# Performance work log

Measured on AMD Instinct MI355X. Metric: run time of the kernel, lower is better.

The kernel has to match this reference:

```python
import jax, jax.numpy as jnp
import numpy as np

F_FEAT = 310   # len(feature_names)
B = 2048       # samples; x has F_FEAT*B elements
H = 32         # sfp_neurons


def _uniform(key, shape, bound):
    return jax.random.uniform(key, shape, jnp.float32, -bound, bound)


def setup_inputs() -> dict:
    key = jax.random.key(0)
    ks = jax.random.split(key, 7)
    x = jax.random.normal(ks[0], (F_FEAT, B), dtype=jnp.float32)
    # Stacked per-feature MLP params (torch Linear default init: U(-1/sqrt(fan_in), +)).
    s1 = 1.0 / np.sqrt(F_FEAT - 1)
    s2 = 1.0 / np.sqrt(H)
    W1 = _uniform(ks[1], (F_FEAT, F_FEAT - 1, H), s1)  # (in, out) layout
    b1 = _uniform(ks[2], (F_FEAT, H), s1)
    W2 = _uniform(ks[3], (F_FEAT, H, H), s2)
    b2 = _uniform(ks[4], (F_FEAT, H), s2)
    W3 = _uniform(ks[5], (F_FEAT, H, H), s2)
    b3 = _uniform(ks[6], (F_FEAT, H), s2)
    return {"x": x, "W1": W1, "b1": b1, "W2": W2, "b2": b2, "W3": W3, "b3": b3}


def reference(x, W1, b1, W2, b2, W3, b3):
    F_, B_ = x.shape
    # Leave-one-out gather: for SFP i, rows [0..i-1, i+1..F-1] of x (feature-major),
    # then the original's view(-1, 1, F-1) reinterprets the flat buffer as (B, F-1).
    idx = jnp.arange(F_ - 1)[None, :]
    idx = idx + (idx >= jnp.arange(F_)[:, None])          # (F, F-1)
    X = x[idx].reshape(F_, B_, F_ - 1)                    # (F, B, F-1) grouped inputs
    h = jax.nn.relu(jnp.einsum('fbk,fkh->fbh', X, W1) + b1[:, None, :])
    h = jax.nn.relu(jnp.einsum('fbh,fhg->fbg', h, W2) + b2[:, None, :])
    h = jax.nn.relu(jnp.einsum('fbh,fhg->fbg', h, W3) + b3[:, None, :])  # (F, B, H)
    # torch.cat of per-SFP .view(-1) == row-major flatten of (F, B, H)
    return h.reshape(-1)
```

## Files before the change

kernel.cpp:

```cpp
#include <hip/hip_runtime.h>

namespace {

constexpr int F_FEAT = 310;
constexpr int KDIM   = 309;
constexpr int BSZ    = 2048;
constexpr int HDIM   = 32;
constexpr int NCH    = 10;
constexpr int NX     = F_FEAT * BSZ;

constexpr int    NBLK8    = NX / 8 + 2;
constexpr size_t CSTR_B   = (size_t)NBLK8 * 16;
constexpr size_t XC_BYTES = CSTR_B * 8;
constexpr size_t W1T_FSTR = 32 * 320 * 2;
constexpr size_t W1T_OFF  = XC_BYTES;
constexpr size_t W2T_OFF  = W1T_OFF + (size_t)F_FEAT * W1T_FSTR;
constexpr size_t WT_FSTR  = 32 * 32 * 2;
constexpr size_t W3T_OFF  = W2T_OFF + (size_t)F_FEAT * WT_FSTR;
constexpr size_t WS_NEED  = W3T_OFF + (size_t)F_FEAT * WT_FSTR;

constexpr int NBX      = (NBLK8 + 255) / 256;
constexpr int CVT_XBLK = NBX * 8;
constexpr int CVT_BLK  = CVT_XBLK + F_FEAT * 6;

typedef __bf16 bf16x8 __attribute__((ext_vector_type(8)));
typedef float  f32x4  __attribute__((ext_vector_type(4)));

#define MFMA(a, b, c) __builtin_amdgcn_mfma_f32_16x16x32_bf16((a), (b), (c), 0, 0, 0)

__global__ __launch_bounds__(256) void cvt_all(
    const float* __restrict__ x,  const float* __restrict__ W1,
    const float* __restrict__ W2, const float* __restrict__ W3,
    char* __restrict__ ws)
{
    __shared__ float tile[64][33];
    const int b = blockIdx.x, tid = threadIdx.x;

    if (b < CVT_XBLK) {
        const int c = b / NBX, mb = b - c * NBX;
        const int m = mb * 256 + tid;
        if (m >= NBLK8) return;
        const int e0 = m * 8 - c;
        bf16x8 v;
        #pragma unroll
        for (int q = 0; q < 8; ++q) {
            const int i = e0 + q;
            v[q] = (__bf16)((i >= 0 && i < NX) ? x[i] : 0.f);
        }
        *(bf16x8*)(ws + (size_t)c * CSTR_B + (size_t)m * 16) = v;
        return;
    }

    const int wb = b - CVT_XBLK;
    const int fi = wb / 6, part = wb - fi * 6;

    if (part < 5) {
        const float* Wg = W1 + (size_t)fi * KDIM * HDIM;
        const int row = tid >> 2;
        const int c8  = (tid & 3) * 8;
        const int k   = part * 64 + row;
        float4 f0 = make_float4(0,0,0,0), f1 = f0;
        if (k < KDIM) {
            f0 = *(const float4*)&Wg[k * HDIM + c8];
            f1 = *(const float4*)&Wg[k * HDIM + c8 + 4];
        }
        tile[row][c8+0] = f0.x; tile[row][c8+1] = f0.y;
        tile[row][c8+2] = f0.z; tile[row][c8+3] = f0.w;
        tile[row][c8+4] = f1.x; tile[row][c8+5] = f1.y;
        tile[row][c8+6] = f1.z; tile[row][c8+7] = f1.w;
        __syncthreads();
        const int h = tid & 31, kq = (tid >> 5) * 8;
        bf16x8 o;
        #pragma unroll
        for (int j = 0; j < 8; ++j) o[j] = (__bf16)tile[kq + j][h];
        const int boff = (h * 640 + part * 128 + kq * 2) ^ ((h & 7) << 4);
        *(bf16x8*)(ws + W1T_OFF + (size_t)fi * W1T_FSTR + (size_t)boff) = o;
    } else {
        const int kl = tid >> 3, h4 = (tid & 7) * 4;
        const int h = tid & 31, kq = (tid >> 5) * 8;
        {
            const float* Wg = W2 + (size_t)fi * HDIM * HDIM;
            float4 f = *(const float4*)&Wg[kl * HDIM + h4];
            tile[kl][h4+0] = f.x; tile[kl][h4+1] = f.y;
            tile[kl][h4+2] = f.z; tile[kl][h4+3] = f.w;
            __syncthreads();
            if (tid < 128) {
                bf16x8 o;
                #pragma unroll
                for (int j = 0; j < 8; ++j) o[j] = (__bf16)tile[kq + j][h];
                *(bf16x8*)(ws + W2T_OFF + (size_t)fi * WT_FSTR + (size_t)(h * 32 + kq) * 2) = o;
            }
            __syncthreads();
        }
        {
            const float* Wg = W3 + (size_t)fi * HDIM * HDIM;
            float4 f = *(const float4*)&Wg[kl * HDIM + h4];
            tile[kl][h4+0] = f.x; tile[kl][h4+1] = f.y;
            tile[kl][h4+2] = f.z; tile[kl][h4+3] = f.w;
            __syncthreads();
            if (tid < 128) {
                bf16x8 o;
                #pragma unroll
                for (int j = 0; j < 8; ++j) o[j] = (__bf16)tile[kq + j][h];
                *(bf16x8*)(ws + W3T_OFF + (size_t)fi * WT_FSTR + (size_t)(h * 32 + kq) * 2) = o;
            }
        }
    }
}

template<bool FAST>
__global__ __launch_bounds__(256, 4) void sfp5(
    const float* __restrict__ x,
    const float* __restrict__ W1, const float* __restrict__ b1,
    const float* __restrict__ W2, const float* __restrict__ b2,
    const float* __restrict__ W3, const float* __restrict__ b3,
    const char* __restrict__ ws, float* __restrict__ out)
{
    __shared__ __attribute__((aligned(16))) __bf16 W1s[32 * 320];
    __shared__ __attribute__((aligned(16))) __bf16 h1s[256 * 40];

    int fi, sb;
    if (FAST) {
        const int xc = blockIdx.x & 7, li = blockIdx.x >> 3;
        const int cnt = (xc < 6) ? 39 : 38;
        const int lf = li >> 3;
        if (lf >= cnt) return;
        fi = ((xc < 6) ? xc * 39 : 234 + (xc - 6) * 38) + lf;
        sb = li & 7;
    } else {
        fi = blockIdx.x >> 3; sb = blockIdx.x & 7;
    }

    const int tid = threadIdx.x, lane = tid & 63, wv = tid >> 6;
    const int l15 = lane & 15, l16 = lane >> 4;
    const int lk8 = l16 * 8, r0 = l16 * 4;
    const int b0 = sb << 8, iB = fi << 11;
    const int mrow = wv * 64;

    int lin[4];
    const char* base[4];
    #pragma unroll
    for (int m = 0; m < 4; ++m) {
        lin[m] = (b0 + mrow + 16 * m + l15) * KDIM + lk8;
        if (FAST) {
            const int c8 = (-lin[m]) & 7;
            base[m] = ws + (size_t)c8 * CSTR_B + (size_t)(lin[m] + c8) * 2;
        } else {
            base[m] = ws;
        }
    }

    auto fragA = [&](const char* bp, int li_) -> bf16x8 {
        if (FAST) {
            if (__builtin_expect((unsigned)(iB - 1 - li_) < 7u, 0)) {
                bf16x8 r;
                #pragma unroll
                for (int q = 0; q < 8; ++q) {
                    int i = li_ + q; i += (i >= iB) ? BSZ : 0;
                    r[q] = *(const __bf16*)(ws + (size_t)i * 2);
                }
                return r;
            }
            return *(const bf16x8*)(bp + ((li_ >= iB) ? 4096 : 0));
        } else {
            bf16x8 r;
            #pragma unroll
            for (int q = 0; q < 8; ++q) {
                int i = li_ + q; i += (i >= iB) ? BSZ : 0;
                i = (i < NX) ? i : (NX - 1);
                r[q] = (__bf16)x[i];
            }
            return r;
        }
    };

    auto fragW1 = [&](int c, int hrow) -> bf16x8 {
        if (FAST) {
            const int boff = (hrow * 640 + c * 64 + l16 * 16) ^ ((hrow & 7) << 4);
            return *(const bf16x8*)((const char*)W1s + boff);
        } else {
            const float* Wg = W1 + (size_t)fi * KDIM * HDIM;
            bf16x8 r;
            #pragma unroll
            for (int q = 0; q < 8; ++q) {
                const int k = c * 32 + lk8 + q;
                r[q] = (__bf16)((k < KDIM) ? Wg[k * HDIM + hrow] : 0.f);
            }
            return r;
        }
    };

    bf16x8 a0[4], a1[4], a2[4];
    #pragma unroll
    for (int m = 0; m < 4; ++m) a0[m] = fragA(base[m], lin[m]);
    #pragma unroll
    for (int m = 0; m < 4; ++m) a1[m] = fragA(base[m] + 64, lin[m] + 32);

    if (FAST) {
        const char* src = ws + W1T_OFF + (size_t)fi * W1T_FSTR;
        #pragma unroll
        for (int i = 0; i < 5; ++i) {
            const int off = i * 4096 + tid * 16;
            *(bf16x8*)((char*)W1s + off) = *(const bf16x8*)(src + off);
        }
        __syncthreads();
    }

    f32x4 acc[4][2];
    #pragma unroll
    for (int m = 0; m < 4; ++m) { acc[m][0] = {0,0,0,0}; acc[m][1] = {0,0,0,0}; }

    bf16x8 w0 = fragW1(0, l15), w1 = fragW1(0, 16 + l15);
    #pragma unroll
    for (int c = 0; c < NCH; ++c) {
        if (c + 2 < NCH) {
            #pragma unroll
            for (int m = 0; m < 4; ++m)
                a2[m] = fragA(base[m] + 64 * (c + 2), lin[m] + 32 * (c + 2));
        }
        bf16x8 nw0, nw1;
        if (c + 1 < NCH) { nw0 = fragW1(c + 1, l15); nw1 = fragW1(c + 1, 16 + l15); }
        #pragma unroll
        for (int m = 0; m < 4; ++m) {
            acc[m][0] = MFMA(a0[m], w0, acc[m][0]);
            acc[m][1] = MFMA(a0[m], w1, acc[m][1]);
        }
        #pragma unroll
        for (int m = 0; m < 4; ++m) { a0[m] = a1[m]; a1[m] = a2[m]; }
        w0 = nw0; w1 = nw1;
    }

    bf16x8 w2a, w2b, w3a, w3b;
    if (FAST) {
        const char* p2 = ws + W2T_OFF + (size_t)fi * WT_FSTR;
        const char* p3 = ws + W3T_OFF + (size_t)fi * WT_FSTR;
        w2a = *(const bf16x8*)(p2 + (size_t)(l15 * 32 + lk8) * 2);
        w2b = *(const bf16x8*)(p2 + (size_t)((16 + l15) * 32 + lk8) * 2);
        w3a = *(const bf16x8*)(p3 + (size_t)(l15 * 32 + lk8) * 2);
        w3b = *(const bf16x8*)(p3 + (size_t)((16 + l15) * 32 + lk8) * 2);
    } else {
        #pragma unroll
        for (int q = 0; q < 8; ++q) {
            const size_t base2 = (size_t)fi * HDIM * HDIM + (lk8 + q) * HDIM;
            w2a[q] = (__bf16)W2[base2 + l15];      w2b[q] = (__bf16)W2[base2 + 16 + l15];
            w3a[q] = (__bf16)W3[base2 + l15];      w3b[q] = (__bf16)W3[base2 + 16 + l15];
        }
    }
    const float b1v0 = b1[fi*HDIM + l15], b1v1 = b1[fi*HDIM + 16 + l15];
    const float b2v0 = b2[fi*HDIM + l15], b2v1 = b2[fi*HDIM + 16 + l15];
    const float b3v0 = b3[fi*HDIM + l15], b3v1 = b3[fi*HDIM + 16 + l15];

    constexpr int LDA = 40;
    #pragma unroll
    for (int m = 0; m < 4; ++m)
        #pragma unroll
        for (int r = 0; r < 4; ++r) {
            float v;
            v = acc[m][0][r] + b1v0; h1s[(mrow + 16*m + r0 + r)*LDA +      l15] = (__bf16)(v > 0.f ? v : 0.f);
            v = acc[m][1][r] + b1v1; h1s[(mrow + 16*m + r0 + r)*LDA + 16 + l15] = (__bf16)(v > 0.f ? v : 0.f);
        }

    const f32x4 z = {0,0,0,0};
    f32x4 c2[4][2];
    #pragma unroll
    for (int m = 0; m < 4; ++m) {
        bf16x8 ha = *(const bf16x8*)&h1s[(mrow + 16*m + l15)*LDA + lk8];
        c2[m][0] = MFMA(ha, w2a, z);
        c2[m][1] = MFMA(ha, w2b, z);
    }
    #pragma unroll
    for (int m = 0; m < 4; ++m)
        #pragma unroll
        for (int r = 0; r < 4; ++r) {
            float v;
            v = c2[m][0][r] + b2v0; h1s[(mrow + 16*m + r0 + r)*LDA +      l15] = (__bf16)(v > 0.f ? v : 0.f);
            v = c2[m][1][r] + b2v1; h1s[(mrow + 16*m + r0 + r)*LDA + 16 + l15] = (__bf16)(v > 0.f ? v : 0.f);
        }

    const size_t orow = (size_t)(fi * BSZ + b0 + mrow);
    #pragma unroll
    for (int m = 0; m < 4; ++m) {
        bf16x8 ha = *(const bf16x8*)&h1s[(mrow + 16*m + l15)*LDA + lk8];
        f32x4 c30 = MFMA(ha, w3a, z);
        f32x4 c31 = MFMA(ha, w3b, z);
        #pragma unroll
        for (int r = 0; r < 4; ++r) {
            float v;
            v = c30[r] + b3v0; out[(orow + 16*m + r0 + r)*HDIM +      l15] = v > 0.f ? v : 0.f;
            v = c31[r] + b3v1; out[(orow + 16*m + r0 + r)*HDIM + 16 + l15] = v > 0.f ? v : 0.f;
        }
    }
}

}

extern "C" void kernel_launch(void* const* d_in, const int* in_sizes, int n_in,
                              void* d_out, int out_size, void* d_ws, size_t ws_size,
                              hipStream_t stream) {
    const float* x  = (const float*)d_in[0];
    const float* W1 = (const float*)d_in[1];
    const float* b1 = (const float*)d_in[2];
    const float* W2 = (const float*)d_in[3];
    const float* b2 = (const float*)d_in[4];
    const float* W3 = (const float*)d_in[5];
    const float* b3 = (const float*)d_in[6];
    float* out = (float*)d_out;
    char* ws = (char*)d_ws;

    const bool fast = (ws != nullptr) && (ws_size >= WS_NEED);
    if (fast) {
        hipLaunchKernelGGL(cvt_all, dim3(CVT_BLK), dim3(256), 0, stream, x, W1, W2, W3, ws);
        hipLaunchKernelGGL((sfp5<true>), dim3(8 * 39 * 8), dim3(256), 0, stream,
                           x, W1, b1, W2, b2, W3, b3, ws, out);
    } else {
        hipLaunchKernelGGL((sfp5<false>), dim3(F_FEAT * 8), dim3(256), 0, stream,
                           x, W1, b1, W2, b2, W3, b3, ws, out);
    }
}
```

Baseline: 71.88 us.

## Hand-schedule layer-1 A loads with inline asm and explicit vmcnt waits

```diff
diff --git a/kernel.cpp b/kernel.cpp
--- a/kernel.cpp
+++ b/kernel.cpp
@@ -25,6 +25,7 @@
 
 typedef __bf16 bf16x8 __attribute__((ext_vector_type(8)));
 typedef float  f32x4  __attribute__((ext_vector_type(4)));
+typedef int    i32x4  __attribute__((ext_vector_type(4)));
 
 #define MFMA(a, b, c) __builtin_amdgcn_mfma_f32_16x16x32_bf16((a), (b), (c), 0, 0, 0)
 
@@ -109,7 +110,7 @@
 }
 
 template<bool FAST>
-__global__ __launch_bounds__(256, 4) void sfp5(
+__global__ __launch_bounds__(256, 4) void sfp6(
     const float* __restrict__ x,
     const float* __restrict__ W1, const float* __restrict__ b1,
     const float* __restrict__ W2, const float* __restrict__ b2,
@@ -119,17 +120,7 @@
     __shared__ __attribute__((aligned(16))) __bf16 W1s[32 * 320];
     __shared__ __attribute__((aligned(16))) __bf16 h1s[256 * 40];
 
-    int fi, sb;
-    if (FAST) {
-        const int xc = blockIdx.x & 7, li = blockIdx.x >> 3;
-        const int cnt = (xc < 6) ? 39 : 38;
-        const int lf = li >> 3;
-        if (lf >= cnt) return;
-        fi = ((xc < 6) ? xc * 39 : 234 + (xc - 6) * 38) + lf;
-        sb = li & 7;
-    } else {
-        fi = blockIdx.x >> 3; sb = blockIdx.x & 7;
-    }
+    const int fi = blockIdx.x >> 3, sb = blockIdx.x & 7;
 
     const int tid = threadIdx.x, lane = tid & 63, wv = tid >> 6;
     const int l15 = lane & 15, l16 = lane >> 4;
@@ -137,42 +128,15 @@
     const int b0 = sb << 8, iB = fi << 11;
     const int mrow = wv * 64;
 
-    int lin[4];
-    const char* base[4];
+    int d[4];
+    unsigned off[4];
     #pragma unroll
     for (int m = 0; m < 4; ++m) {
-        lin[m] = (b0 + mrow + 16 * m + l15) * KDIM + lk8;
-        if (FAST) {
-            const int c8 = (-lin[m]) & 7;
-            base[m] = ws + (size_t)c8 * CSTR_B + (size_t)(lin[m] + c8) * 2;
-        } else {
-            base[m] = ws;
-        }
-    }
-
-    auto fragA = [&](const char* bp, int li_) -> bf16x8 {
-        if (FAST) {
-            if (__builtin_expect((unsigned)(iB - 1 - li_) < 7u, 0)) {
-                bf16x8 r;
-                #pragma unroll
-                for (int q = 0; q < 8; ++q) {
-                    int i = li_ + q; i += (i >= iB) ? BSZ : 0;
-                    r[q] = *(const __bf16*)(ws + (size_t)i * 2);
-                }
-                return r;
-            }
-            return *(const bf16x8*)(bp + ((li_ >= iB) ? 4096 : 0));
-        } else {
-            bf16x8 r;
-            #pragma unroll
-            for (int q = 0; q < 8; ++q) {
-                int i = li_ + q; i += (i >= iB) ? BSZ : 0;
-                i = (i < NX) ? i : (NX - 1);
-                r[q] = (__bf16)x[i];
-            }
-            return r;
-        }
-    };
+        const int lin = (b0 + mrow + 16 * m + l15) * KDIM + lk8;
+        d[m] = iB - lin;
+        const int c8 = (-lin) & 7;
+        off[m] = (unsigned)((size_t)c8 * CSTR_B) + (unsigned)(lin + c8) * 2u;
+    }
 
     auto fragW1 = [&](int c, int hrow) -> bf16x8 {
         if (FAST) {
@@ -190,44 +154,94 @@
         }
     };
 
-    bf16x8 a0[4], a1[4], a2[4];
-    #pragma unroll
-    for (int m = 0; m < 4; ++m) a0[m] = fragA(base[m], lin[m]);
-    #pragma unroll
-    for (int m = 0; m < 4; ++m) a1[m] = fragA(base[m] + 64, lin[m] + 32);
-
-    if (FAST) {
-        const char* src = ws + W1T_OFF + (size_t)fi * W1T_FSTR;
-        #pragma unroll
-        for (int i = 0; i < 5; ++i) {
-            const int off = i * 4096 + tid * 16;
-            *(bf16x8*)((char*)W1s + off) = *(const bf16x8*)(src + off);
+    f32x4 acc[4][2];
+    #pragma unroll
+    for (int m = 0; m < 4; ++m) { acc[m][0] = {0,0,0,0}; acc[m][1] = {0,0,0,0}; }
+
+    if constexpr (FAST) {
+        {
+            const char* src = ws + W1T_OFF + (size_t)fi * W1T_FSTR;
+            #pragma unroll
+            for (int i = 0; i < 5; ++i) {
+                const int o = i * 4096 + tid * 16;
+                *(bf16x8*)((char*)W1s + o) = *(const bf16x8*)(src + o);
+            }
         }
         __syncthreads();
-    }
-
-    f32x4 acc[4][2];
-    #pragma unroll
-    for (int m = 0; m < 4; ++m) { acc[m][0] = {0,0,0,0}; acc[m][1] = {0,0,0,0}; }
-
-    bf16x8 w0 = fragW1(0, l15), w1 = fragW1(0, 16 + l15);
-    #pragma unroll
-    for (int c = 0; c < NCH; ++c) {
-        if (c + 2 < NCH) {
-            #pragma unroll
-            for (int m = 0; m < 4; ++m)
-                a2[m] = fragA(base[m] + 64 * (c + 2), lin[m] + 32 * (c + 2));
-        }
-        bf16x8 nw0, nw1;
-        if (c + 1 < NCH) { nw0 = fragW1(c + 1, l15); nw1 = fragW1(c + 1, 16 + l15); }
-        #pragma unroll
-        for (int m = 0; m < 4; ++m) {
-            acc[m][0] = MFMA(a0[m], w0, acc[m][0]);
-            acc[m][1] = MFMA(a0[m], w1, acc[m][1]);
-        }
-        #pragma unroll
-        for (int m = 0; m < 4; ++m) { a0[m] = a1[m]; a1[m] = a2[m]; }
-        w0 = nw0; w1 = nw1;
+
+        bf16x8 ab[3][4];
+
+        auto issueLd = [&](int c) {
+            #pragma unroll
+            for (int m = 0; m < 4; ++m) {
+                const unsigned sel = (32 * c >= d[m]) ? 4096u : 0u;
+                const char* p = ws + (off[m] + (unsigned)(64 * c) + sel);
+                i32x4 r;
+                asm volatile("global_load_dwordx4 %0, %1, off" : "=v"(r) : "v"(p));
+                ab[c % 3][m] = __builtin_bit_cast(bf16x8, r);
+            }
+        };
+
+        issueLd(0);
+        issueLd(1);
+
+        #pragma unroll
+        for (int c = 0; c < NCH; ++c) {
+            if (c + 2 < NCH) issueLd(c + 2);
+            bf16x8 w0 = fragW1(c, l15), w1 = fragW1(c, 16 + l15);
+            if (c <= 7)      asm volatile("s_waitcnt vmcnt(8)");
+            else if (c == 8) asm volatile("s_waitcnt vmcnt(4)");
+            else             asm volatile("s_waitcnt vmcnt(0)");
+            __builtin_amdgcn_sched_barrier(0);
+
+            const bool h0 = (unsigned)(d[0] - 32*c - 1) < 7u;
+            const bool h1 = (unsigned)(d[1] - 32*c - 1) < 7u;
+            const bool h2 = (unsigned)(d[2] - 32*c - 1) < 7u;
+            const bool h3 = (unsigned)(d[3] - 32*c - 1) < 7u;
+            if (__any(h0 | h1 | h2 | h3)) {
+                #pragma unroll
+                for (int m = 0; m < 4; ++m) {
+                    const bool hm = (unsigned)(d[m] - 32*c - 1) < 7u;
+                    if (hm) {
+                        const int li_ = iB - d[m] + 32*c;
+                        bf16x8 r;
+                        #pragma unroll
+                        for (int q = 0; q < 8; ++q) {
+                            int i = li_ + q; i += (i >= iB) ? BSZ : 0;
+                            r[q] = *(const __bf16*)(ws + (size_t)i * 2);
+                        }
+                        ab[c % 3][m] = r;
+                    }
+                }
+            }
+
+            #pragma unroll
+            for (int m = 0; m < 4; ++m) {
+                acc[m][0] = MFMA(ab[c % 3][m], w0, acc[m][0]);
+                acc[m][1] = MFMA(ab[c % 3][m], w1, acc[m][1]);
+            }
+        }
+        __builtin_amdgcn_sched_barrier(0);
+    } else {
+        auto fragA = [&](int li_) -> bf16x8 {
+            bf16x8 r;
+            #pragma unroll
+            for (int q = 0; q < 8; ++q) {
+                int i = li_ + q; i += (i >= iB) ? BSZ : 0;
+                i = (i < NX) ? i : (NX - 1);
+                r[q] = (__bf16)x[i];
+            }
+            return r;
+        };
+        for (int c = 0; c < NCH; ++c) {
+            bf16x8 w0 = fragW1(c, l15), w1 = fragW1(c, 16 + l15);
+            #pragma unroll
+            for (int m = 0; m < 4; ++m) {
+                bf16x8 a = fragA(iB - d[m] + 32 * c);
+                acc[m][0] = MFMA(a, w0, acc[m][0]);
+                acc[m][1] = MFMA(a, w1, acc[m][1]);
+            }
+        }
     }
 
     bf16x8 w2a, w2b, w3a, w3b;
@@ -310,10 +324,10 @@
     const bool fast = (ws != nullptr) && (ws_size >= WS_NEED);
     if (fast) {
         hipLaunchKernelGGL(cvt_all, dim3(CVT_BLK), dim3(256), 0, stream, x, W1, W2, W3, ws);
-        hipLaunchKernelGGL((sfp5<true>), dim3(8 * 39 * 8), dim3(256), 0, stream,
+        hipLaunchKernelGGL((sfp6<true>), dim3(F_FEAT * 8), dim3(256), 0, stream,
                            x, W1, b1, W2, b2, W3, b3, ws, out);
     } else {
-        hipLaunchKernelGGL((sfp5<false>), dim3(F_FEAT * 8), dim3(256), 0, stream,
+        hipLaunchKernelGGL((sfp6<false>), dim3(F_FEAT * 8), dim3(256), 0, stream,
                            x, W1, b1, W2, b2, W3, b3, ws, out);
     }
 }
```

After: 75.09 us. +4.5%, slower.
